# Optimization experiments

Hardware: AMD Instinct MI355X
Metric: run time of the kernel (lower is better)

The kernel has to match this reference:

```python
import jax, jax.numpy as jnp
import numpy as np

N_NODES = 500_000
N_EDGES = 16_000_000
V_DIM, E_DIM = 2, 3  # V_DIM + E_DIM == 5 == MLP input dim


def setup_inputs() -> dict:
    key = jax.random.key(0)
    k1, k2, k3, kw1, kw2, kw3 = jax.random.split(key, 6)
    vertex_attr = jax.random.normal(k1, (N_NODES, V_DIM), dtype=jnp.float32)
    edge_index = jax.random.randint(k2, (2, N_EDGES), 0, N_NODES, dtype=jnp.int64)
    edge_attr = jax.random.normal(k3, (N_EDGES, E_DIM), dtype=jnp.float32)
    # init_weights: uniform [0,1) weights, bias = 0.01 (torch Linear: y = x @ W.T + b)
    W1 = jax.random.uniform(kw1, (50, 5), dtype=jnp.float32)
    b1 = jnp.full((50,), 0.01, dtype=jnp.float32)
    W2 = jax.random.uniform(kw2, (20, 50), dtype=jnp.float32)
    b2 = jnp.full((20,), 0.01, dtype=jnp.float32)
    W3 = jax.random.uniform(kw3, (1, 20), dtype=jnp.float32)
    b3 = jnp.full((1,), 0.01, dtype=jnp.float32)
    return {"vertex_attr": vertex_attr, "edge_index": edge_index, "edge_attr": edge_attr,
            "W1": W1, "b1": b1, "W2": W2, "b2": b2, "W3": W3, "b3": b3}


def reference(vertex_attr, edge_index, edge_attr, W1, b1, W2, b2, W3, b3):
    n = vertex_attr.shape[0]
    # edge aggregation: sum edge features onto target nodes (edge_index[1])
    agg_edges = jax.ops.segment_sum(edge_attr, edge_index[1], num_segments=n)  # [N, 3]
    x = jnp.concatenate([vertex_attr, agg_edges], axis=1)  # [N, 5]
    h = jax.nn.relu(x @ W1.T + b1)
    h = jax.nn.relu(h @ W2.T + b2)
    return h @ W3.T + b3  # [N, 1]
```

## Files before the change

kernel.cpp:

```cpp
#include <hip/hip_runtime.h>
#include <stdint.h>


#define SB_SHIFT 11
#define SB_NODES 2048
#define NSB 256
#define CHUNK 4096
#define TB 512
#define THREADS 256
#define SPLIT 4

typedef float vf4 __attribute__((ext_vector_type(4)));
typedef int vi4 __attribute__((ext_vector_type(4)));

__global__ __launch_bounds__(THREADS) void hist_kernel(
    const int* __restrict__ tgt, int n_edges, int* __restrict__ counts) {
  __shared__ int h[NSB];
  for (int i = threadIdx.x; i < NSB; i += THREADS) h[i] = 0;
  __syncthreads();
  int w = blockIdx.x;
  int base = w * CHUNK;
  int end = min(base + CHUNK, n_edges);
  if (end - base == CHUNK) {
    const vi4* tp = (const vi4*)(tgt + base);
    for (int i = threadIdx.x; i < CHUNK / 4; i += THREADS) {
      vi4 t4 = tp[i];
      atomicAdd(&h[t4.x >> SB_SHIFT], 1);
      atomicAdd(&h[t4.y >> SB_SHIFT], 1);
      atomicAdd(&h[t4.z >> SB_SHIFT], 1);
      atomicAdd(&h[t4.w >> SB_SHIFT], 1);
    }
  } else {
    for (int e = base + (int)threadIdx.x; e < end; e += THREADS)
      atomicAdd(&h[tgt[e] >> SB_SHIFT], 1);
  }
  __syncthreads();
  int* row = counts + (size_t)w * NSB;
  for (int i = threadIdx.x; i < NSB; i += THREADS) row[i] = h[i];
}

__global__ __launch_bounds__(THREADS) void scan1_kernel(
    int* __restrict__ counts, int nw, int* __restrict__ row_total) {
  __shared__ int part[THREADS];
  int b = blockIdx.x;
  int per = (nw + THREADS - 1) / THREADS;
  int w0 = threadIdx.x * per;
  int w1 = min(w0 + per, nw);
  int s = 0;
  for (int w = w0; w < w1; ++w) s += counts[(size_t)w * NSB + b];
  part[threadIdx.x] = s;
  __syncthreads();
  for (int off = 1; off < THREADS; off <<= 1) {
    int v = (threadIdx.x >= off) ? part[threadIdx.x - off] : 0;
    __syncthreads();
    part[threadIdx.x] += v;
    __syncthreads();
  }
  int run = part[threadIdx.x] - s;
  for (int w = w0; w < w1; ++w) {
    int v = counts[(size_t)w * NSB + b];
    counts[(size_t)w * NSB + b] = run;
    run += v;
  }
  if (threadIdx.x == THREADS - 1) row_total[b] = part[THREADS - 1];
}

__global__ __launch_bounds__(THREADS) void scan2_kernel(
    const int* __restrict__ row_total, int* __restrict__ sb_base) {
  __shared__ int part[THREADS];
  int v = row_total[threadIdx.x];
  part[threadIdx.x] = v;
  __syncthreads();
  for (int off = 1; off < THREADS; off <<= 1) {
    int u = (threadIdx.x >= off) ? part[threadIdx.x - off] : 0;
    __syncthreads();
    part[threadIdx.x] += u;
    __syncthreads();
  }
  sb_base[threadIdx.x] = part[threadIdx.x] - v;
}

__global__ __launch_bounds__(TB) void bin_kernel(
    const int* __restrict__ tgt, const float* __restrict__ eattr, int n_edges,
    const int* __restrict__ rowpref, const int* __restrict__ sb_base,
    float* __restrict__ rec3, unsigned short* __restrict__ ids) {
  __shared__ float eattr_s[CHUNK * 3];
  __shared__ unsigned short inv[CHUNK];
  __shared__ int h[NSB];
  __shared__ int excl[NSB];
  __shared__ int wb[NSB];
  __shared__ int part[NSB];

  int tid = threadIdx.x;
  int w = blockIdx.x;
  int base = w * CHUNK;
  int end = min(base + CHUNK, n_edges);
  int m = end - base;
  bool full = (m == CHUNK);

  for (int i = tid; i < NSB; i += TB) h[i] = 0;
  __syncthreads();

  vi4 tc[CHUNK / 4 / TB];
  if (full) {
    const vi4* tp = (const vi4*)(tgt + base);
#pragma unroll
    for (int k = 0; k < CHUNK / 4 / TB; ++k) {
      tc[k] = tp[tid + k * TB];
      atomicAdd(&h[tc[k].x >> SB_SHIFT], 1);
      atomicAdd(&h[tc[k].y >> SB_SHIFT], 1);
      atomicAdd(&h[tc[k].z >> SB_SHIFT], 1);
      atomicAdd(&h[tc[k].w >> SB_SHIFT], 1);
    }
  } else {
    for (int e = base + tid; e < end; e += TB)
      atomicAdd(&h[tgt[e] >> SB_SHIFT], 1);
  }

  {
    const float* src = eattr + (size_t)base * 3;
    int nd = m * 3;
    int nv = nd >> 2;
    const vf4* s4 = (const vf4*)src;
    for (int i = tid; i < nv; i += TB) {
      vf4 v = __builtin_nontemporal_load(s4 + i);
      *(vf4*)(&eattr_s[i * 4]) = v;
    }
    for (int i = (nv << 2) + tid; i < nd; i += TB) eattr_s[i] = src[i];
  }
  __syncthreads();

  int myh = 0;
  if (tid < NSB) {
    myh = h[tid];
    part[tid] = myh;
  }
  __syncthreads();
  for (int off = 1; off < NSB; off <<= 1) {
    int v = 0;
    if (tid < NSB && tid >= off) v = part[tid - off];
    __syncthreads();
    if (tid < NSB) part[tid] += v;
    __syncthreads();
  }
  if (tid < NSB) {
    excl[tid] = part[tid] - myh;
    wb[tid] = sb_base[tid] + rowpref[(size_t)w * NSB + tid];
  }
  __syncthreads();

  for (int i = tid; i < NSB; i += TB) h[i] = excl[i];
  __syncthreads();
  if (full) {
#pragma unroll
    for (int k = 0; k < CHUNK / 4 / TB; ++k) {
      int e0 = (tid + k * TB) * 4;
      int sp;
      sp = atomicAdd(&h[tc[k].x >> SB_SHIFT], 1);
      inv[sp] = (unsigned short)e0;
      sp = atomicAdd(&h[tc[k].y >> SB_SHIFT], 1);
      inv[sp] = (unsigned short)(e0 + 1);
      sp = atomicAdd(&h[tc[k].z >> SB_SHIFT], 1);
      inv[sp] = (unsigned short)(e0 + 2);
      sp = atomicAdd(&h[tc[k].w >> SB_SHIFT], 1);
      inv[sp] = (unsigned short)(e0 + 3);
    }
  } else {
    for (int e = base + tid; e < end; e += TB) {
      int sp = atomicAdd(&h[tgt[e] >> SB_SHIFT], 1);
      inv[sp] = (unsigned short)(e - base);
    }
  }
  __syncthreads();

  for (int sidx = tid; sidx < m; sidx += TB) {
    int el = inv[sidx];
    int t = tgt[base + el];
    int bk = t >> SB_SHIFT;
    int slot = wb[bk] + (sidx - excl[bk]);
    float a0 = eattr_s[el * 3 + 0];
    float a1 = eattr_s[el * 3 + 1];
    float a2 = eattr_s[el * 3 + 2];
    size_t o = (size_t)slot * 3;
    rec3[o + 0] = a0;
    rec3[o + 1] = a1;
    rec3[o + 2] = a2;
    ids[slot] = (unsigned short)(t & (SB_NODES - 1));
  }
}

__global__ __launch_bounds__(TB) void agg_kernel(
    const float* __restrict__ rec3, const unsigned short* __restrict__ ids,
    const int* __restrict__ sb_base, const int* __restrict__ row_total,
    float* __restrict__ partials, size_t pstride) {
  __shared__ float acc[SB_NODES * 3];
  int tid = threadIdx.x;
  for (int i = tid; i < SB_NODES * 3; i += TB) acc[i] = 0.f;
  __syncthreads();
  int b = blockIdx.x / SPLIT;
  int j = blockIdx.x % SPLIT;
  int cnt = row_total[b];
  int rbase = sb_base[b];
  int q = (cnt + SPLIT - 1) / SPLIT;
  int lo = j * q;
  int hi = min(cnt, lo + q);
  for (int i = lo + tid; i < hi; i += TB) {
    size_t s = (size_t)(rbase + i);
    float r0 = rec3[s * 3 + 0];
    float r1 = rec3[s * 3 + 1];
    float r2 = rec3[s * 3 + 2];
    int local = ids[s];
    atomicAdd(&acc[local * 3 + 0], r0);
    atomicAdd(&acc[local * 3 + 1], r1);
    atomicAdd(&acc[local * 3 + 2], r2);
  }
  __syncthreads();
  float* pj = partials + (size_t)j * pstride + (((size_t)b << SB_SHIFT) * 3);
  for (int i = tid; i < SB_NODES * 3; i += TB) pj[i] = acc[i];
}

__global__ __launch_bounds__(THREADS) void mlp_reduce_kernel(
    const float* __restrict__ va, const float* __restrict__ partials,
    size_t pstride, const float* __restrict__ W1, const float* __restrict__ b1,
    const float* __restrict__ W2, const float* __restrict__ b2,
    const float* __restrict__ W3, const float* __restrict__ b3,
    float* __restrict__ out, int n) {
  int i = blockIdx.x * THREADS + threadIdx.x;
  if (i >= n) return;
  float a0 = 0.f, a1 = 0.f, a2 = 0.f;
#pragma unroll
  for (int j = 0; j < SPLIT; ++j) {
    const float* p = partials + (size_t)j * pstride + (size_t)i * 3;
    a0 += p[0];
    a1 += p[1];
    a2 += p[2];
  }
  float x[5];
  float2 v = ((const float2*)va)[i];
  x[0] = v.x;
  x[1] = v.y;
  x[2] = a0;
  x[3] = a1;
  x[4] = a2;

  float h1[50];
#pragma unroll
  for (int j = 0; j < 50; ++j) {
    float s = b1[j];
#pragma unroll
    for (int k = 0; k < 5; ++k) s = fmaf(W1[j * 5 + k], x[k], s);
    h1[j] = fmaxf(s, 0.0f);
  }
  float h2[20];
#pragma unroll
  for (int j = 0; j < 20; ++j) {
    float s = b2[j];
#pragma unroll
    for (int k = 0; k < 50; ++k) s = fmaf(W2[j * 50 + k], h1[k], s);
    h2[j] = fmaxf(s, 0.0f);
  }
  float s = b3[0];
#pragma unroll
  for (int k = 0; k < 20; ++k) s = fmaf(W3[k], h2[k], s);
  out[i] = s;
}

__global__ __launch_bounds__(THREADS) void scatter_dev_kernel(
    const int* __restrict__ tgt, const float* __restrict__ eattr,
    float* __restrict__ agg, int n_edges) {
  int e = blockIdx.x * blockDim.x + threadIdx.x;
  if (e >= n_edges) return;
  int d = tgt[e];
  atomicAdd(&agg[d * 4 + 0], eattr[(size_t)e * 3 + 0]);
  atomicAdd(&agg[d * 4 + 1], eattr[(size_t)e * 3 + 1]);
  atomicAdd(&agg[d * 4 + 2], eattr[(size_t)e * 3 + 2]);
}

__global__ __launch_bounds__(THREADS) void mlp_table_kernel(
    const float* __restrict__ va, const vf4* __restrict__ table,
    const float* __restrict__ W1, const float* __restrict__ b1,
    const float* __restrict__ W2, const float* __restrict__ b2,
    const float* __restrict__ W3, const float* __restrict__ b3,
    float* __restrict__ out, int n) {
  int i = blockIdx.x * blockDim.x + threadIdx.x;
  if (i >= n) return;
  float x[5];
  float2 v = ((const float2*)va)[i];
  vf4 t = table[i];
  x[0] = v.x; x[1] = v.y; x[2] = t.x; x[3] = t.y; x[4] = t.z;
  float h1[50];
#pragma unroll
  for (int j = 0; j < 50; ++j) {
    float s = b1[j];
#pragma unroll
    for (int k = 0; k < 5; ++k) s = fmaf(W1[j * 5 + k], x[k], s);
    h1[j] = fmaxf(s, 0.0f);
  }
  float h2[20];
#pragma unroll
  for (int j = 0; j < 20; ++j) {
    float s = b2[j];
#pragma unroll
    for (int k = 0; k < 50; ++k) s = fmaf(W2[j * 50 + k], h1[k], s);
    h2[j] = fmaxf(s, 0.0f);
  }
  float s = b3[0];
#pragma unroll
  for (int k = 0; k < 20; ++k) s = fmaf(W3[k], h2[k], s);
  out[i] = s;
}

extern "C" void kernel_launch(void* const* d_in, const int* in_sizes, int n_in,
                              void* d_out, int out_size, void* d_ws, size_t ws_size,
                              hipStream_t stream) {
  const float* vertex_attr = (const float*)d_in[0];
  const int* edge_index = (const int*)d_in[1];
  const float* edge_attr = (const float*)d_in[2];
  const float* W1 = (const float*)d_in[3];
  const float* b1 = (const float*)d_in[4];
  const float* W2 = (const float*)d_in[5];
  const float* b2 = (const float*)d_in[6];
  const float* W3 = (const float*)d_in[7];
  const float* b3 = (const float*)d_in[8];
  float* out = (float*)d_out;

  const int n_nodes = in_sizes[0] / 2;
  const int n_edges = in_sizes[2] / 3;
  const int* tgt = edge_index + n_edges;

  const int nsb_rt = (n_nodes + SB_NODES - 1) >> SB_SHIFT;
  const int nw = (n_edges + CHUNK - 1) / CHUNK;
  const size_t Np = (size_t)nsb_rt << SB_SHIFT;
  const size_t pstride = Np * 3;

  char* ws = (char*)d_ws;
  size_t o = 0;
  float* rec3 = (float*)(ws + o);
  o += (size_t)n_edges * 3 * sizeof(float);
  o = (o + 255) & ~(size_t)255;
  unsigned short* ids = (unsigned short*)(ws + o);
  o += (size_t)n_edges * sizeof(unsigned short);
  o = (o + 255) & ~(size_t)255;
  int* row_total = (int*)(ws + o);
  o += NSB * sizeof(int);
  int* sb_base = (int*)(ws + o);
  o += NSB * sizeof(int);
  o = (o + 255) & ~(size_t)255;
  int* counts = (int*)(ws + o);
  o += (size_t)nw * NSB * sizeof(int);
  o = (o + 255) & ~(size_t)255;
  float* partials = (float*)(ws + o);
  o += (size_t)SPLIT * pstride * sizeof(float);
  const size_t need = o;

  if (nsb_rt <= NSB && ws_size >= need) {
    hist_kernel<<<nw, THREADS, 0, stream>>>(tgt, n_edges, counts);
    scan1_kernel<<<NSB, THREADS, 0, stream>>>(counts, nw, row_total);
    scan2_kernel<<<1, THREADS, 0, stream>>>(row_total, sb_base);
    bin_kernel<<<nw, TB, 0, stream>>>(tgt, edge_attr, n_edges, counts, sb_base,
                                      rec3, ids);
    agg_kernel<<<nsb_rt * SPLIT, TB, 0, stream>>>(rec3, ids, sb_base,
                                                  row_total, partials, pstride);
    mlp_reduce_kernel<<<(n_nodes + THREADS - 1) / THREADS, THREADS, 0,
                        stream>>>(vertex_attr, partials, pstride, W1, b1, W2,
                                  b2, W3, b3, out, n_nodes);
  } else {
    vf4* table = (vf4*)ws;
    hipMemsetAsync(table, 0, (size_t)n_nodes * sizeof(vf4), stream);
    const int nblk = (n_edges + THREADS - 1) / THREADS;
    scatter_dev_kernel<<<nblk, THREADS, 0, stream>>>(tgt, edge_attr,
                                                     (float*)table, n_edges);
    mlp_table_kernel<<<(n_nodes + THREADS - 1) / THREADS, THREADS, 0, stream>>>(
        vertex_attr, table, W1, b1, W2, b2, W3, b3, out, n_nodes);
  }
}
```

Measured before the change: 737.1 us.

## Transpose per-chunk bin counts and align bins for vectorized aggregation loads

```diff
diff --git a/kernel.cpp b/kernel.cpp
--- a/kernel.cpp
+++ b/kernel.cpp
@@ -12,9 +12,11 @@
 
 typedef float vf4 __attribute__((ext_vector_type(4)));
 typedef int vi4 __attribute__((ext_vector_type(4)));
+typedef unsigned int vu2 __attribute__((ext_vector_type(2)));
 
 __global__ __launch_bounds__(THREADS) void hist_kernel(
-    const int* __restrict__ tgt, int n_edges, int* __restrict__ counts) {
+    const int* __restrict__ tgt, int n_edges, int* __restrict__ counts_T,
+    int nwpad) {
   __shared__ int h[NSB];
   for (int i = threadIdx.x; i < NSB; i += THREADS) h[i] = 0;
   __syncthreads();
@@ -35,19 +37,20 @@
       atomicAdd(&h[tgt[e] >> SB_SHIFT], 1);
   }
   __syncthreads();
-  int* row = counts + (size_t)w * NSB;
-  for (int i = threadIdx.x; i < NSB; i += THREADS) row[i] = h[i];
+  for (int i = threadIdx.x; i < NSB; i += THREADS)
+    counts_T[(size_t)i * nwpad + w] = h[i];
 }
 
 __global__ __launch_bounds__(THREADS) void scan1_kernel(
-    int* __restrict__ counts, int nw, int* __restrict__ row_total) {
+    int* __restrict__ counts_T, int nw, int nwpad, int* __restrict__ row_total) {
   __shared__ int part[THREADS];
   int b = blockIdx.x;
+  int* row = counts_T + (size_t)b * nwpad;
   int per = (nw + THREADS - 1) / THREADS;
   int w0 = threadIdx.x * per;
   int w1 = min(w0 + per, nw);
   int s = 0;
-  for (int w = w0; w < w1; ++w) s += counts[(size_t)w * NSB + b];
+  for (int w = w0; w < w1; ++w) s += row[w];
   part[threadIdx.x] = s;
   __syncthreads();
   for (int off = 1; off < THREADS; off <<= 1) {
@@ -58,8 +61,8 @@
   }
   int run = part[threadIdx.x] - s;
   for (int w = w0; w < w1; ++w) {
-    int v = counts[(size_t)w * NSB + b];
-    counts[(size_t)w * NSB + b] = run;
+    int v = row[w];
+    row[w] = run;
     run += v;
   }
   if (threadIdx.x == THREADS - 1) row_total[b] = part[THREADS - 1];
@@ -68,7 +71,7 @@
 __global__ __launch_bounds__(THREADS) void scan2_kernel(
     const int* __restrict__ row_total, int* __restrict__ sb_base) {
   __shared__ int part[THREADS];
-  int v = row_total[threadIdx.x];
+  int v = (row_total[threadIdx.x] + 3) & ~3;
   part[threadIdx.x] = v;
   __syncthreads();
   for (int off = 1; off < THREADS; off <<= 1) {
@@ -82,7 +85,8 @@
 
 __global__ __launch_bounds__(TB) void bin_kernel(
     const int* __restrict__ tgt, const float* __restrict__ eattr, int n_edges,
-    const int* __restrict__ rowpref, const int* __restrict__ sb_base,
+    const int* __restrict__ rowpref_T, int nwpad,
+    const int* __restrict__ sb_base,
     float* __restrict__ rec3, unsigned short* __restrict__ ids) {
   __shared__ float eattr_s[CHUNK * 3];
   __shared__ unsigned short inv[CHUNK];
@@ -145,7 +149,7 @@
   }
   if (tid < NSB) {
     excl[tid] = part[tid] - myh;
-    wb[tid] = sb_base[tid] + rowpref[(size_t)w * NSB + tid];
+    wb[tid] = sb_base[tid] + rowpref_T[(size_t)tid * nwpad + w];
   }
   __syncthreads();
 
@@ -201,18 +205,46 @@
   int j = blockIdx.x % SPLIT;
   int cnt = row_total[b];
   int rbase = sb_base[b];
-  int q = (cnt + SPLIT - 1) / SPLIT;
+  int q = (((cnt + SPLIT - 1) / SPLIT) + 3) & ~3;
   int lo = j * q;
   int hi = min(cnt, lo + q);
-  for (int i = lo + tid; i < hi; i += TB) {
-    size_t s = (size_t)(rbase + i);
-    float r0 = rec3[s * 3 + 0];
-    float r1 = rec3[s * 3 + 1];
-    float r2 = rec3[s * 3 + 2];
-    int local = ids[s];
-    atomicAdd(&acc[local * 3 + 0], r0);
-    atomicAdd(&acc[local * 3 + 1], r1);
-    atomicAdd(&acc[local * 3 + 2], r2);
+  int len = hi - lo;
+  if (len > 0) {
+    int nq = len >> 2;
+    for (int k = tid; k < nq; k += TB) {
+      int s0 = rbase + lo + (k << 2);
+      const vf4* rp = (const vf4*)(rec3 + (size_t)s0 * 3);
+      vf4 r0 = rp[0];
+      vf4 r1 = rp[1];
+      vf4 r2 = rp[2];
+      vu2 u = *(const vu2*)(ids + s0);
+      int l0 = u.x & 0xFFFF;
+      int l1 = u.x >> 16;
+      int l2 = u.y & 0xFFFF;
+      int l3 = u.y >> 16;
+      atomicAdd(&acc[l0 * 3 + 0], r0.x);
+      atomicAdd(&acc[l0 * 3 + 1], r0.y);
+      atomicAdd(&acc[l0 * 3 + 2], r0.z);
+      atomicAdd(&acc[l1 * 3 + 0], r0.w);
+      atomicAdd(&acc[l1 * 3 + 1], r1.x);
+      atomicAdd(&acc[l1 * 3 + 2], r1.y);
+      atomicAdd(&acc[l2 * 3 + 0], r1.z);
+      atomicAdd(&acc[l2 * 3 + 1], r1.w);
+      atomicAdd(&acc[l2 * 3 + 2], r2.x);
+      atomicAdd(&acc[l3 * 3 + 0], r2.y);
+      atomicAdd(&acc[l3 * 3 + 1], r2.z);
+      atomicAdd(&acc[l3 * 3 + 2], r2.w);
+    }
+    for (int i = lo + (nq << 2) + tid; i < hi; i += TB) {
+      size_t s = (size_t)(rbase + i);
+      float r0 = rec3[s * 3 + 0];
+      float r1 = rec3[s * 3 + 1];
+      float r2 = rec3[s * 3 + 2];
+      int local = ids[s];
+      atomicAdd(&acc[local * 3 + 0], r0);
+      atomicAdd(&acc[local * 3 + 1], r1);
+      atomicAdd(&acc[local * 3 + 2], r2);
+    }
   }
   __syncthreads();
   float* pj = partials + (size_t)j * pstride + (((size_t)b << SB_SHIFT) * 3);
@@ -330,35 +362,37 @@
 
   const int nsb_rt = (n_nodes + SB_NODES - 1) >> SB_SHIFT;
   const int nw = (n_edges + CHUNK - 1) / CHUNK;
+  const int nwpad = nw;
   const size_t Np = (size_t)nsb_rt << SB_SHIFT;
   const size_t pstride = Np * 3;
+  const int rec_cap = n_edges + 4 * NSB;
 
   char* ws = (char*)d_ws;
   size_t o = 0;
   float* rec3 = (float*)(ws + o);
-  o += (size_t)n_edges * 3 * sizeof(float);
+  o += (size_t)rec_cap * 3 * sizeof(float);
   o = (o + 255) & ~(size_t)255;
   unsigned short* ids = (unsigned short*)(ws + o);
-  o += (size_t)n_edges * sizeof(unsigned short);
+  o += (size_t)rec_cap * sizeof(unsigned short);
   o = (o + 255) & ~(size_t)255;
   int* row_total = (int*)(ws + o);
   o += NSB * sizeof(int);
   int* sb_base = (int*)(ws + o);
   o += NSB * sizeof(int);
   o = (o + 255) & ~(size_t)255;
-  int* counts = (int*)(ws + o);
-  o += (size_t)nw * NSB * sizeof(int);
+  int* counts_T = (int*)(ws + o);
+  o += (size_t)NSB * nwpad * sizeof(int);
   o = (o + 255) & ~(size_t)255;
   float* partials = (float*)(ws + o);
   o += (size_t)SPLIT * pstride * sizeof(float);
   const size_t need = o;
 
   if (nsb_rt <= NSB && ws_size >= need) {
-    hist_kernel<<<nw, THREADS, 0, stream>>>(tgt, n_edges, counts);
-    scan1_kernel<<<NSB, THREADS, 0, stream>>>(counts, nw, row_total);
+    hist_kernel<<<nw, THREADS, 0, stream>>>(tgt, n_edges, counts_T, nwpad);
+    scan1_kernel<<<NSB, THREADS, 0, stream>>>(counts_T, nw, nwpad, row_total);
     scan2_kernel<<<1, THREADS, 0, stream>>>(row_total, sb_base);
-    bin_kernel<<<nw, TB, 0, stream>>>(tgt, edge_attr, n_edges, counts, sb_base,
-                                      rec3, ids);
+    bin_kernel<<<nw, TB, 0, stream>>>(tgt, edge_attr, n_edges, counts_T, nwpad,
+                                      sb_base, rec3, ids);
     agg_kernel<<<nsb_rt * SPLIT, TB, 0, stream>>>(rec3, ids, sb_base,
                                                   row_total, partials, pstride);
     mlp_reduce_kernel<<<(n_nodes + THREADS - 1) / THREADS, THREADS, 0,
```

Result: no change. 734.0 us (-0.4%).
